# Performance work log

Measured on AMD Instinct MI355X. Metric: run time of the kernel, lower is better.

## Reference

```python
import jax, jax.numpy as jnp
import numpy as np

B, N, F, H, HEADS = 2, 256, 64, 64, 4
C = HEADS * H  # n_coefficients (coefficients_mlp is Identity => must equal n_heads*hidden)
EPS = 1e-5
INF = 1e5


def _lin(key, fan_in, fan_out, bias=True):
    k1, k2 = jax.random.split(key)
    w = jax.random.normal(k1, (fan_in, fan_out), jnp.float32) * (1.0 / np.sqrt(fan_in))
    if bias:
        b = jax.random.normal(k2, (fan_out,), jnp.float32) * 0.01
        return w, b
    return w


def setup_inputs() -> dict:
    key = jax.random.key(0)
    ks = jax.random.split(key, 16)
    inp = dict(
        h=jax.random.normal(ks[0], (B, N, F), jnp.float32),
        x=jax.random.normal(ks[1], (B, N, 3), jnp.float32),
        v=jax.random.normal(ks[2], (B, N, 3), jnp.float32),
    )
    inp['edge_w1'], inp['edge_b1'] = _lin(ks[3], 2 * F + 1, H)
    inp['edge_w2'], inp['edge_b2'] = _lin(ks[4], H, H)
    inp['sem_w'], inp['sem_b'] = _lin(ks[5], H, HEADS)
    inp['post_w1'], inp['post_b1'] = _lin(ks[6], C, H)
    inp['post_w2'], inp['post_b2'] = _lin(ks[7], H, H)
    inp['node_w1'], inp['node_b1'] = _lin(ks[8], C + H + F, H)
    inp['node_w2'], inp['node_b2'] = _lin(ks[9], H, F)
    inp['vel_w1'], inp['vel_b1'] = _lin(ks[10], F, H)
    inp['vel_w2'] = _lin(ks[11], H, 1, bias=False) * 0.001  # xavier gain=0.001 analogue
    inp['vmix_w'] = _lin(ks[12], C, 1, bias=False)[:, 0]
    inp['log_gamma'] = -jnp.log(jnp.linspace(1.0, 5.0, HEADS)).astype(jnp.float32)
    return inp


def reference(h, x, v, edge_w1, edge_b1, edge_w2, edge_b2, sem_w, sem_b,
              post_w1, post_b1, post_w2, post_b2, node_w1, node_b1,
              node_w2, node_b2, vel_w1, vel_b1, vel_w2, vmix_w, log_gamma):
    silu = jax.nn.silu
    n = h.shape[-2]
    eye = jnp.eye(n, dtype=h.dtype)[:, :, None]  # [N,N,1] diagonal mask

    # pairwise geometry: entry [i,j] = x_j - x_i
    x_minus_xt = x[..., None, :, :] - x[..., :, None, :]                # [B,N,N,3]
    x_norm = jnp.sqrt((x_minus_xt ** 2).sum(-1, keepdims=True) + EPS)   # [B,N,N,1]

    # pairwise node-feature concat (h_j, h_i) + distance -> edge MLP
    h_j = jnp.broadcast_to(h[..., None, :, :], (B, n, n, F))
    h_i = jnp.broadcast_to(h[..., :, None, :], (B, n, n, F))
    h_cat = jnp.concatenate([h_j, h_i, x_norm], axis=-1)                # [B,N,N,2F+1]
    h_e_mtx = silu(silu(h_cat @ edge_w1 + edge_b1) @ edge_w2 + edge_b2)  # [B,N,N,H]

    # euclidean attention: softmin over j of gamma*dist, diagonal masked out
    dist = (x_norm + INF * eye) * jnp.exp(log_gamma)                    # [B,N,N,heads]
    euclid_att = jax.nn.softmax(-dist, axis=-2)
    # semantic attention: LeakyReLU(0.2) logits, diagonal masked, softmax over j
    sem = jax.nn.leaky_relu(h_e_mtx @ sem_w + sem_b, 0.2) - INF * eye
    sem_att = jax.nn.softmax(sem, axis=-2)
    comb_att = jax.nn.softmax(euclid_att * sem_att, axis=-2)            # [B,N,N,heads]

    # attention-weighted edge features, flattened over (H, heads)
    h_e_att = (h_e_mtx[..., :, None] * comb_att[..., None, :]).reshape(B, n, n, C)

    # spatial attention (coefficients_mlp is Identity)
    unit = x_minus_xt / (x_norm + EPS)                                  # [B,N,N,3]
    # combinations.mean(dim=-3) without materializing [B,N,N,C,3]
    comb_sum = jnp.einsum('bijc,bijd->bicd', h_e_att, unit) / n         # [B,N,C,3]
    comb_norm = (comb_sum ** 2).sum(-1)                                 # [B,N,C]
    h_comb = silu(silu(comb_norm @ post_w1 + post_b1) @ post_w2 + post_b2)

    # delta_v = mean_j (v_mixing over C of combinations)
    delta_v = jnp.einsum('bijc,c,bijd->bid', h_e_att, vmix_w, unit) / n  # [B,N,3]

    h_agg = h_e_att.sum(axis=-2)                                        # sum over j -> [B,N,C]
    out = jnp.concatenate([h, h_agg, h_comb], axis=-1)
    out = silu(silu(out @ node_w1 + node_b1) @ node_w2 + node_b2)
    h_new = h + out                                                     # residual

    # coordinate / velocity update
    v_scale = silu(h_new @ vel_w1 + vel_b1) @ vel_w2                    # [B,N,1]
    v_new = delta_v + v_scale * v
    x_new = x + v_new
    return h_new, x_new, v_new
```

## Files before the change

### kernel.cpp

```cpp
#include <hip/hip_runtime.h>
#include <hip/hip_bf16.h>
#include <math.h>

#define EPSV 1e-5f
#define INFV 1e5f

typedef short bf16x8 __attribute__((ext_vector_type(8)));
typedef float f32x4 __attribute__((ext_vector_type(4)));

__device__ __forceinline__ float rcp_f(float x) { return __builtin_amdgcn_rcpf(x); }
__device__ __forceinline__ float silu_f(float v) { return v * rcp_f(1.0f + __expf(-v)); }

__device__ __forceinline__ unsigned short f2bf(float f) {
  unsigned int u = __float_as_uint(f);
  u = (u + 0x7fffu + ((u >> 16) & 1u)) >> 16;
  return (unsigned short)u;
}
__device__ __forceinline__ float bf2f(unsigned short h) {
  return __uint_as_float(((unsigned int)h) << 16);
}
__device__ __forceinline__ unsigned int pkbf(float a, float b) {
  float2 f2; f2.x = a; f2.y = b;
  __hip_bfloat162 t = __float22bfloat162_rn(f2);
  unsigned int u;
  __builtin_memcpy(&u, &t, 4);
  return u;
}

__device__ __forceinline__ float4 br4(float4 v, int op, float4* sc) {
  const int tid = threadIdx.x;
#pragma unroll
  for (int off = 32; off >= 1; off >>= 1) {
    float ox = __shfl_xor(v.x, off);
    float oy = __shfl_xor(v.y, off);
    float oz = __shfl_xor(v.z, off);
    float ow = __shfl_xor(v.w, off);
    if (op) { v.x = fmaxf(v.x, ox); v.y = fmaxf(v.y, oy); v.z = fmaxf(v.z, oz); v.w = fmaxf(v.w, ow); }
    else    { v.x += ox; v.y += oy; v.z += oz; v.w += ow; }
  }
  if ((tid & 63) == 0) sc[tid >> 6] = v;
  __syncthreads();
  float4 r0 = sc[0], r1 = sc[1], r2 = sc[2], r3 = sc[3];
  if (op) {
    v.x = fmaxf(fmaxf(r0.x, r1.x), fmaxf(r2.x, r3.x));
    v.y = fmaxf(fmaxf(r0.y, r1.y), fmaxf(r2.y, r3.y));
    v.z = fmaxf(fmaxf(r0.z, r1.z), fmaxf(r2.z, r3.z));
    v.w = fmaxf(fmaxf(r0.w, r1.w), fmaxf(r2.w, r3.w));
  } else {
    v.x = r0.x + r1.x + r2.x + r3.x;
    v.y = r0.y + r1.y + r2.y + r3.y;
    v.z = r0.z + r1.z + r2.z + r3.z;
    v.w = r0.w + r1.w + r2.w + r3.w;
  }
  __syncthreads();
  return v;
}

__device__ __forceinline__ void gemm64(const unsigned short* TH, const unsigned short* E2T,
                                       int w, int l15, int quad, f32x4 acc[4][4]) {
#pragma unroll
  for (int tr = 0; tr < 4; ++tr)
#pragma unroll
    for (int tc = 0; tc < 4; ++tc)
      acc[tr][tc] = (f32x4){0.f, 0.f, 0.f, 0.f};
#pragma unroll
  for (int ms = 0; ms < 64; ms += 32) {
    bf16x8 af[4], bfr[4];
#pragma unroll
    for (int tr = 0; tr < 4; ++tr)
      af[tr] = *reinterpret_cast<const bf16x8*>(&TH[(64 * w + 16 * tr + l15) * 72 + ms + quad * 8]);
#pragma unroll
    for (int tc = 0; tc < 4; ++tc)
      bfr[tc] = *reinterpret_cast<const bf16x8*>(&E2T[(16 * tc + l15) * 72 + ms + quad * 8]);
#pragma unroll
    for (int tr = 0; tr < 4; ++tr)
#pragma unroll
      for (int tc = 0; tc < 4; ++tc)
        acc[tr][tc] = __builtin_amdgcn_mfma_f32_16x16x32_bf16(af[tr], bfr[tc], acc[tr][tc], 0, 0, 0);
  }
}

__global__ __launch_bounds__(256, 3) void k_all(
    const float* __restrict__ h, const float* __restrict__ x, const float* __restrict__ v,
    const float* __restrict__ ew1, const float* __restrict__ eb1,
    const float* __restrict__ ew2, const float* __restrict__ eb2,
    const float* __restrict__ semw, const float* __restrict__ semb,
    const float* __restrict__ pw1, const float* __restrict__ pb1,
    const float* __restrict__ pw2, const float* __restrict__ pb2,
    const float* __restrict__ nw1, const float* __restrict__ nb1,
    const float* __restrict__ nw2, const float* __restrict__ nb2,
    const float* __restrict__ vw1, const float* __restrict__ vb1,
    const float* __restrict__ vw2, const float* __restrict__ vmix,
    const float* __restrict__ lgam, float* __restrict__ out) {

  __shared__ __align__(16) unsigned short TH[256 * 72];
  __shared__ __align__(16) char E2u[9216];
  __shared__ __align__(16) float4 unit_l[256];
  __shared__ float addk[64];
  __shared__ float w1dk[64];
  __shared__ __align__(16) float bms[256];

  unsigned short* E2T = (unsigned short*)E2u;
  float*  sd    = (float*)E2u;
  float4* cat_l = (float4*)E2u;
  float*  cn_l  = (float*)(E2u + 4096);
  float*  hag_l = (float*)(E2u + 5120);
  float4* sc    = (float4*)(E2u + 8192);
  float*  dvs   = (float*)(E2u + 8320);
  float* tmp = (float*)TH;
  float* m1s = (float*)TH + 256;
  float* hnw = (float*)TH + 320;
  float* nin = (float*)TH + 384;

  const int bi  = blockIdx.x;
  const int i   = bi & 255;
  const int b0  = bi & ~255;
  const int tid = threadIdx.x;
  const int j   = tid;
  const int bj  = b0 | j;

  const float xi0 = x[bi * 3 + 0], xi1 = x[bi * 3 + 1], xi2 = x[bi * 3 + 2];
  const float dx = x[bj * 3 + 0] - xi0;
  const float dy = x[bj * 3 + 1] - xi1;
  const float dz = x[bj * 3 + 2] - xi2;
  const float dn = sqrtf(dx * dx + dy * dy + dz * dz + EPSV);
  const float invn = rcp_f(dn + EPSV);
  const float ux = dx * invn, uy = dy * invn, uz = dz * invn;
  unit_l[j] = make_float4(ux, uy, uz, dn);

  {
    const float4* hb4 = reinterpret_cast<const float4*>(h + (size_t)b0 * 64);
#pragma unroll
    for (int q = 0; q < 16; ++q) {
      int idx = q * 256 + tid;
      float4 f4 = hb4[idx];
      int row = idx >> 4, c4 = idx & 15;
      uint2 pk;
      pk.x = pkbf(f4.x, f4.y);
      pk.y = pkbf(f4.z, f4.w);
      *reinterpret_cast<uint2*>(&TH[row * 72 + c4 * 4]) = pk;
    }
  }
#pragma unroll
  for (int q = 0; q < 16; ++q) {
    int idx = q * 256 + tid;
    E2T[(idx & 63) * 72 + (idx >> 6)] = f2bf(ew1[idx]);
  }
  {
    int s = tid >> 6, k = tid & 63;
    const float* hrow = h + (size_t)bi * 64;
    float bp = 0.f;
#pragma unroll
    for (int f2 = 0; f2 < 16; ++f2) {
      int f = s * 16 + f2;
      bp += hrow[f] * ew1[(64 + f) * 64 + k];
    }
    bms[s * 64 + k] = bp;
  }
  __syncthreads();
  if (tid < 64) {
    addk[tid] = eb1[tid] + bms[tid] + bms[64 + tid] + bms[128 + tid] + bms[192 + tid];
    w1dk[tid] = ew1[128 * 64 + tid];
  }

  const int lid  = tid & 63;
  const int w    = tid >> 6;
  const int l15  = lid & 15;
  const int quad = lid >> 4;

  f32x4 acc[4][4];
  gemm64(TH, E2T, w, l15, quad, acc);
  __syncthreads();

#pragma unroll
  for (int tc = 0; tc < 4; ++tc) {
    float ak = addk[16 * tc + l15];
    float wd = w1dk[16 * tc + l15];
#pragma unroll
    for (int tr = 0; tr < 4; ++tr)
#pragma unroll
      for (int r = 0; r < 4; ++r) {
        int row = 64 * w + 16 * tr + quad * 4 + r;
        float val = silu_f(acc[tr][tc][r] + ak + unit_l[row].w * wd);
        TH[row * 72 + 16 * tc + l15] = f2bf(val);
      }
  }
#pragma unroll
  for (int q = 0; q < 16; ++q) {
    int idx = q * 256 + tid;
    E2T[(idx & 63) * 72 + (idx >> 6)] = f2bf(ew2[idx]);
  }
  __syncthreads();

  gemm64(TH, E2T, w, l15, quad, acc);
  __syncthreads();

#pragma unroll
  for (int tc = 0; tc < 4; ++tc) {
    float b2 = eb2[16 * tc + l15];
#pragma unroll
    for (int tr = 0; tr < 4; ++tr)
#pragma unroll
      for (int r = 0; r < 4; ++r) {
        int row = 64 * w + 16 * tr + quad * 4 + r;
        TH[row * 72 + 16 * tc + l15] = f2bf(silu_f(acc[tr][tc][r] + b2));
      }
  }
#pragma unroll
  for (int q = 0; q < 2; ++q) {
    int idx = q * 256 + tid;
    int n = idx >> 6, kk = idx & 63;
    float wv = (n < 4) ? semw[kk * 4 + n] : vmix[kk * 4 + (n - 4)];
    E2T[n * 72 + kk] = f2bf(wv);
  }
  __syncthreads();

  f32x4 acc3[4];
  {
#pragma unroll
    for (int tr = 0; tr < 4; ++tr) acc3[tr] = (f32x4){0.f, 0.f, 0.f, 0.f};
#pragma unroll
    for (int ms = 0; ms < 64; ms += 32) {
      bf16x8 b3 = *reinterpret_cast<const bf16x8*>(&E2T[l15 * 72 + ms + quad * 8]);
#pragma unroll
      for (int tr = 0; tr < 4; ++tr) {
        bf16x8 a3 = *reinterpret_cast<const bf16x8*>(&TH[(64 * w + 16 * tr + l15) * 72 + ms + quad * 8]);
        acc3[tr] = __builtin_amdgcn_mfma_f32_16x16x32_bf16(a3, b3, acc3[tr], 0, 0, 0);
      }
    }
  }
  __syncthreads();
  if (l15 < 8) {
#pragma unroll
    for (int tr = 0; tr < 4; ++tr)
#pragma unroll
      for (int r = 0; r < 4; ++r)
        sd[(64 * w + 16 * tr + quad * 4 + r) * 8 + l15] = acc3[tr][r];
  }
  __syncthreads();

  float4 s01 = *reinterpret_cast<const float4*>(sd + j * 8);
  float4 s23 = *reinterpret_cast<const float4*>(sd + j * 8 + 4);
  float4 sbv = *reinterpret_cast<const float4*>(semb);
  const float diag = (j == i) ? INFV : 0.0f;
  float4 sl;
  sl.x = s01.x + sbv.x; sl.y = s01.y + sbv.y; sl.z = s01.z + sbv.z; sl.w = s01.w + sbv.w;
  sl.x = ((sl.x > 0.f) ? sl.x : 0.2f * sl.x) - diag;
  sl.y = ((sl.y > 0.f) ? sl.y : 0.2f * sl.y) - diag;
  sl.z = ((sl.z > 0.f) ? sl.z : 0.2f * sl.z) - diag;
  sl.w = ((sl.w > 0.f) ? sl.w : 0.2f * sl.w) - diag;

  float4 lg = *reinterpret_cast<const float4*>(lgam);
  const float dni = dn + diag;
  float4 e_eu = make_float4(__expf(-dni * __expf(lg.x)), __expf(-dni * __expf(lg.y)),
                            __expf(-dni * __expf(lg.z)), __expf(-dni * __expf(lg.w)));

  float4 M = br4(sl, 1, sc);
  float4 e_sem = make_float4(__expf(sl.x - M.x), __expf(sl.y - M.y),
                             __expf(sl.z - M.z), __expf(sl.w - M.w));

  float4 a8 = e_eu, b8 = e_sem;
#pragma unroll
  for (int off = 32; off >= 1; off >>= 1) {
    a8.x += __shfl_xor(a8.x, off); a8.y += __shfl_xor(a8.y, off);
    a8.z += __shfl_xor(a8.z, off); a8.w += __shfl_xor(a8.w, off);
    b8.x += __shfl_xor(b8.x, off); b8.y += __shfl_xor(b8.y, off);
    b8.z += __shfl_xor(b8.z, off); b8.w += __shfl_xor(b8.w, off);
  }
  if ((tid & 63) == 0) { sc[tid >> 6] = a8; sc[4 + (tid >> 6)] = b8; }
  __syncthreads();
  float4 Se, Ss;
  {
    float4 r0 = sc[0], r1 = sc[1], r2 = sc[2], r3 = sc[3];
    Se = make_float4(r0.x + r1.x + r2.x + r3.x, r0.y + r1.y + r2.y + r3.y,
                     r0.z + r1.z + r2.z + r3.z, r0.w + r1.w + r2.w + r3.w);
    float4 s0 = sc[4], s1 = sc[5], s2 = sc[6], s3 = sc[7];
    Ss = make_float4(s0.x + s1.x + s2.x + s3.x, s0.y + s1.y + s2.y + s3.y,
                     s0.z + s1.z + s2.z + s3.z, s0.w + s1.w + s2.w + s3.w);
  }
  __syncthreads();

  float4 p = make_float4((e_eu.x * rcp_f(Se.x)) * (e_sem.x * rcp_f(Ss.x)),
                         (e_eu.y * rcp_f(Se.y)) * (e_sem.y * rcp_f(Ss.y)),
                         (e_eu.z * rcp_f(Se.z)) * (e_sem.z * rcp_f(Ss.z)),
                         (e_eu.w * rcp_f(Se.w)) * (e_sem.w * rcp_f(Ss.w)));
  float4 ep = make_float4(__expf(p.x), __expf(p.y), __expf(p.z), __expf(p.w));
  float4 Sp = br4(ep, 0, sc);
  float4 catt = make_float4(ep.x * rcp_f(Sp.x), ep.y * rcp_f(Sp.y),
                            ep.z * rcp_f(Sp.z), ep.w * rcp_f(Sp.w));
  cat_l[j] = catt;

  float s = catt.x * s23.x + catt.y * s23.y + catt.z * s23.z + catt.w * s23.w;
  float4 dv = br4(make_float4(s * ux, s * uy, s * uz, 0.f), 0, sc);
  if (j == 0) {
    const float inv = 1.0f / 256.0f;
    dvs[0] = dv.x * inv; dvs[1] = dv.y * inv; dvs[2] = dv.z * inv;
  }

  {
    const int kk = lid & 15;
    const int jq = lid >> 4;
    const int k  = 16 * w + kk;
    float agg[4] = {0.f, 0.f, 0.f, 0.f};
    float ax[4]  = {0.f, 0.f, 0.f, 0.f};
    float ay[4]  = {0.f, 0.f, 0.f, 0.f};
    float az[4]  = {0.f, 0.f, 0.f, 0.f};
#pragma unroll 4
    for (int jr2 = 0; jr2 < 64; ++jr2) {
      int jj = jq * 64 + ((jr2 + 4 * jq) & 63);
      float hev = bf2f(TH[jj * 72 + k]);
      float4 ca = cat_l[jj];
      float4 u  = unit_l[jj];
      float w0 = hev * ca.x, w1 = hev * ca.y, w2 = hev * ca.z, w3 = hev * ca.w;
      agg[0] += w0; agg[1] += w1; agg[2] += w2; agg[3] += w3;
      ax[0] += w0 * u.x; ay[0] += w0 * u.y; az[0] += w0 * u.z;
      ax[1] += w1 * u.x; ay[1] += w1 * u.y; az[1] += w1 * u.z;
      ax[2] += w2 * u.x; ay[2] += w2 * u.y; az[2] += w2 * u.z;
      ax[3] += w3 * u.x; ay[3] += w3 * u.y; az[3] += w3 * u.z;
    }
#pragma unroll
    for (int off = 16; off <= 32; off <<= 1) {
#pragma unroll
      for (int hd = 0; hd < 4; ++hd) {
        agg[hd] += __shfl_xor(agg[hd], off);
        ax[hd]  += __shfl_xor(ax[hd], off);
        ay[hd]  += __shfl_xor(ay[hd], off);
        az[hd]  += __shfl_xor(az[hd], off);
      }
    }
    if (jq == 0) {
      const float inv = 1.0f / 256.0f;
#pragma unroll
      for (int hd = 0; hd < 4; ++hd) {
        float cx = ax[hd] * inv, cy = ay[hd] * inv, cz = az[hd] * inv;
        cn_l[k * 4 + hd]  = cx * cx + cy * cy + cz * cz;
        hag_l[k * 4 + hd] = agg[hd];
      }
    }
  }
  __syncthreads();

  const int k = tid & 63;
  {
    float a = 0.f;
    for (int m2 = 0; m2 < 64; ++m2) {
      int m = w * 64 + m2;
      a += cn_l[m] * pw1[m * 64 + k];
    }
    tmp[tid] = a;
  }
  __syncthreads();
  if (tid < 64) m1s[tid] = silu_f(pb1[tid] + tmp[tid] + tmp[64 + tid] + tmp[128 + tid] + tmp[192 + tid]);
  __syncthreads();
  {
    float a = 0.f;
#pragma unroll
    for (int m2 = 0; m2 < 16; ++m2) {
      int m = w * 16 + m2;
      a += m1s[m] * pw2[m * 64 + k];
    }
    float hgv = hag_l[tid];
    __syncthreads();
    tmp[tid] = a;
    nin[64 + tid] = hgv;
  }
  __syncthreads();
  if (tid < 64) {
    nin[tid] = h[(size_t)bi * 64 + tid];
    nin[320 + tid] = silu_f(pb2[tid] + tmp[tid] + tmp[64 + tid] + tmp[128 + tid] + tmp[192 + tid]);
  }
  __syncthreads();
  {
    float a = 0.f;
    for (int m2 = 0; m2 < 96; ++m2) {
      int m = w * 96 + m2;
      a += nin[m] * nw1[m * 64 + k];
    }
    __syncthreads();
    tmp[tid] = a;
  }
  __syncthreads();
  if (tid < 64) m1s[tid] = silu_f(nb1[tid] + tmp[tid] + tmp[64 + tid] + tmp[128 + tid] + tmp[192 + tid]);
  __syncthreads();
  {
    float a = 0.f;
#pragma unroll
    for (int m2 = 0; m2 < 16; ++m2) {
      int m = w * 16 + m2;
      a += m1s[m] * nw2[m * 64 + k];
    }
    __syncthreads();
    tmp[tid] = a;
  }
  __syncthreads();
  if (tid < 64) {
    float hn = h[(size_t)bi * 64 + tid] +
               silu_f(nb2[tid] + tmp[tid] + tmp[64 + tid] + tmp[128 + tid] + tmp[192 + tid]);
    out[(size_t)bi * 64 + tid] = hn;
    hnw[tid] = hn;
  }
  __syncthreads();
  {
    float a = 0.f;
#pragma unroll
    for (int m2 = 0; m2 < 16; ++m2) {
      int m = w * 16 + m2;
      a += hnw[m] * vw1[m * 64 + k];
    }
    __syncthreads();
    tmp[tid] = a;
  }
  __syncthreads();
  if (tid < 64) {
    float vh = silu_f(vb1[tid] + tmp[tid] + tmp[64 + tid] + tmp[128 + tid] + tmp[192 + tid]) * vw2[tid];
#pragma unroll
    for (int off = 32; off >= 1; off >>= 1) vh += __shfl_xor(vh, off);
    if (tid == 0) {
#pragma unroll
      for (int d = 0; d < 3; ++d) {
        float vn = dvs[d] + vh * v[bi * 3 + d];
        out[32768 + bi * 3 + d] = x[bi * 3 + d] + vn;
        out[34304 + bi * 3 + d] = vn;
      }
    }
  }
}

extern "C" void kernel_launch(void* const* d_in, const int* in_sizes, int n_in,
                              void* d_out, int out_size, void* d_ws, size_t ws_size,
                              hipStream_t stream) {
  const float* h    = (const float*)d_in[0];
  const float* x    = (const float*)d_in[1];
  const float* v    = (const float*)d_in[2];
  const float* ew1  = (const float*)d_in[3];
  const float* eb1  = (const float*)d_in[4];
  const float* ew2  = (const float*)d_in[5];
  const float* eb2  = (const float*)d_in[6];
  const float* semw = (const float*)d_in[7];
  const float* semb = (const float*)d_in[8];
  const float* pw1  = (const float*)d_in[9];
  const float* pb1  = (const float*)d_in[10];
  const float* pw2  = (const float*)d_in[11];
  const float* pb2  = (const float*)d_in[12];
  const float* nw1  = (const float*)d_in[13];
  const float* nb1  = (const float*)d_in[14];
  const float* nw2  = (const float*)d_in[15];
  const float* nb2  = (const float*)d_in[16];
  const float* vw1  = (const float*)d_in[17];
  const float* vb1  = (const float*)d_in[18];
  const float* vw2  = (const float*)d_in[19];
  const float* vmix = (const float*)d_in[20];
  const float* lgam = (const float*)d_in[21];
  float* out = (float*)d_out;

  k_all<<<512, 256, 0, stream>>>(h, x, v, ew1, eb1, ew2, eb2, semw, semb,
                                 pw1, pb1, pw2, pb2, nw1, nb1, nw2, nb2,
                                 vw1, vb1, vw2, vmix, lgam, out);
}
```

Before: 125.3 us.

## Cut block barriers in softmax reductions and run tail MLPs on one wave

The semantic softmax no longer subtracts a block-wide max, which removes one full block reduction. Each remaining reduction gets its own scratch slot, so several __syncthreads calls can be dropped, including the one between the sem-logit MFMA and the scatter into shared memory. The post, node and velocity MLP tail now runs entirely on wave 0 with no block barriers, instead of being split across four waves with partial-sum merges. The risks are possible exp overflow for large logits, a shared-memory overlap race between the relocated sd buffer and E2T reads, and a longer serial tail on a single wave.

```diff
diff --git a/kernel.cpp b/kernel.cpp
--- a/kernel.cpp
+++ b/kernel.cpp
@@ -25,35 +25,6 @@
   unsigned int u;
   __builtin_memcpy(&u, &t, 4);
   return u;
-}
-
-__device__ __forceinline__ float4 br4(float4 v, int op, float4* sc) {
-  const int tid = threadIdx.x;
-#pragma unroll
-  for (int off = 32; off >= 1; off >>= 1) {
-    float ox = __shfl_xor(v.x, off);
-    float oy = __shfl_xor(v.y, off);
-    float oz = __shfl_xor(v.z, off);
-    float ow = __shfl_xor(v.w, off);
-    if (op) { v.x = fmaxf(v.x, ox); v.y = fmaxf(v.y, oy); v.z = fmaxf(v.z, oz); v.w = fmaxf(v.w, ow); }
-    else    { v.x += ox; v.y += oy; v.z += oz; v.w += ow; }
-  }
-  if ((tid & 63) == 0) sc[tid >> 6] = v;
-  __syncthreads();
-  float4 r0 = sc[0], r1 = sc[1], r2 = sc[2], r3 = sc[3];
-  if (op) {
-    v.x = fmaxf(fmaxf(r0.x, r1.x), fmaxf(r2.x, r3.x));
-    v.y = fmaxf(fmaxf(r0.y, r1.y), fmaxf(r2.y, r3.y));
-    v.z = fmaxf(fmaxf(r0.z, r1.z), fmaxf(r2.z, r3.z));
-    v.w = fmaxf(fmaxf(r0.w, r1.w), fmaxf(r2.w, r3.w));
-  } else {
-    v.x = r0.x + r1.x + r2.x + r3.x;
-    v.y = r0.y + r1.y + r2.y + r3.y;
-    v.z = r0.z + r1.z + r2.z + r3.z;
-    v.w = r0.w + r1.w + r2.w + r3.w;
-  }
-  __syncthreads();
-  return v;
 }
 
 __device__ __forceinline__ void gemm64(const unsigned short* TH, const unsigned short* E2T,
@@ -94,23 +65,21 @@
     const float* __restrict__ lgam, float* __restrict__ out) {
 
   __shared__ __align__(16) unsigned short TH[256 * 72];
-  __shared__ __align__(16) char E2u[9216];
+  __shared__ __align__(16) char E2u[9472];
   __shared__ __align__(16) float4 unit_l[256];
   __shared__ float addk[64];
   __shared__ float w1dk[64];
   __shared__ __align__(16) float bms[256];
 
   unsigned short* E2T = (unsigned short*)E2u;
-  float*  sd    = (float*)E2u;
+  float*  sd    = (float*)(E2u + 1280);
   float4* cat_l = (float4*)E2u;
   float*  cn_l  = (float*)(E2u + 4096);
   float*  hag_l = (float*)(E2u + 5120);
-  float4* sc    = (float4*)(E2u + 8192);
-  float*  dvs   = (float*)(E2u + 8320);
-  float* tmp = (float*)TH;
-  float* m1s = (float*)TH + 256;
-  float* hnw = (float*)TH + 320;
-  float* nin = (float*)TH + 384;
+  float4* scS = (float4*)bms;
+  float4* scP = (float4*)bms + 8;
+  float4* scD = (float4*)bms + 12;
+  float*  dvs = bms + 64;
 
   const int bi  = blockIdx.x;
   const int i   = bi & 255;
@@ -229,7 +198,6 @@
       }
     }
   }
-  __syncthreads();
   if (l15 < 8) {
 #pragma unroll
     for (int tr = 0; tr < 4; ++tr)
@@ -254,10 +222,7 @@
   const float dni = dn + diag;
   float4 e_eu = make_float4(__expf(-dni * __expf(lg.x)), __expf(-dni * __expf(lg.y)),
                             __expf(-dni * __expf(lg.z)), __expf(-dni * __expf(lg.w)));
-
-  float4 M = br4(sl, 1, sc);
-  float4 e_sem = make_float4(__expf(sl.x - M.x), __expf(sl.y - M.y),
-                             __expf(sl.z - M.z), __expf(sl.w - M.w));
+  float4 e_sem = make_float4(__expf(sl.x), __expf(sl.y), __expf(sl.z), __expf(sl.w));
 
   float4 a8 = e_eu, b8 = e_sem;
 #pragma unroll
@@ -267,34 +232,55 @@
     b8.x += __shfl_xor(b8.x, off); b8.y += __shfl_xor(b8.y, off);
     b8.z += __shfl_xor(b8.z, off); b8.w += __shfl_xor(b8.w, off);
   }
-  if ((tid & 63) == 0) { sc[tid >> 6] = a8; sc[4 + (tid >> 6)] = b8; }
+  if (lid == 0) { scS[w] = a8; scS[4 + w] = b8; }
   __syncthreads();
   float4 Se, Ss;
   {
-    float4 r0 = sc[0], r1 = sc[1], r2 = sc[2], r3 = sc[3];
+    float4 r0 = scS[0], r1 = scS[1], r2 = scS[2], r3 = scS[3];
     Se = make_float4(r0.x + r1.x + r2.x + r3.x, r0.y + r1.y + r2.y + r3.y,
                      r0.z + r1.z + r2.z + r3.z, r0.w + r1.w + r2.w + r3.w);
-    float4 s0 = sc[4], s1 = sc[5], s2 = sc[6], s3 = sc[7];
+    float4 s0 = scS[4], s1 = scS[5], s2 = scS[6], s3 = scS[7];
     Ss = make_float4(s0.x + s1.x + s2.x + s3.x, s0.y + s1.y + s2.y + s3.y,
                      s0.z + s1.z + s2.z + s3.z, s0.w + s1.w + s2.w + s3.w);
   }
-  __syncthreads();
 
   float4 p = make_float4((e_eu.x * rcp_f(Se.x)) * (e_sem.x * rcp_f(Ss.x)),
                          (e_eu.y * rcp_f(Se.y)) * (e_sem.y * rcp_f(Ss.y)),
                          (e_eu.z * rcp_f(Se.z)) * (e_sem.z * rcp_f(Ss.z)),
                          (e_eu.w * rcp_f(Se.w)) * (e_sem.w * rcp_f(Ss.w)));
   float4 ep = make_float4(__expf(p.x), __expf(p.y), __expf(p.z), __expf(p.w));
-  float4 Sp = br4(ep, 0, sc);
+  float4 sp8 = ep;
+#pragma unroll
+  for (int off = 32; off >= 1; off >>= 1) {
+    sp8.x += __shfl_xor(sp8.x, off); sp8.y += __shfl_xor(sp8.y, off);
+    sp8.z += __shfl_xor(sp8.z, off); sp8.w += __shfl_xor(sp8.w, off);
+  }
+  if (lid == 0) scP[w] = sp8;
+  __syncthreads();
+  float4 Sp;
+  {
+    float4 r0 = scP[0], r1 = scP[1], r2 = scP[2], r3 = scP[3];
+    Sp = make_float4(r0.x + r1.x + r2.x + r3.x, r0.y + r1.y + r2.y + r3.y,
+                     r0.z + r1.z + r2.z + r3.z, r0.w + r1.w + r2.w + r3.w);
+  }
   float4 catt = make_float4(ep.x * rcp_f(Sp.x), ep.y * rcp_f(Sp.y),
                             ep.z * rcp_f(Sp.z), ep.w * rcp_f(Sp.w));
   cat_l[j] = catt;
 
   float s = catt.x * s23.x + catt.y * s23.y + catt.z * s23.z + catt.w * s23.w;
-  float4 dv = br4(make_float4(s * ux, s * uy, s * uz, 0.f), 0, sc);
+  float dvx = s * ux, dvy = s * uy, dvz = s * uz;
+#pragma unroll
+  for (int off = 32; off >= 1; off >>= 1) {
+    dvx += __shfl_xor(dvx, off); dvy += __shfl_xor(dvy, off); dvz += __shfl_xor(dvz, off);
+  }
+  if (lid == 0) scD[w] = make_float4(dvx, dvy, dvz, 0.f);
+  __syncthreads();
   if (j == 0) {
+    float4 r0 = scD[0], r1 = scD[1], r2 = scD[2], r3 = scD[3];
     const float inv = 1.0f / 256.0f;
-    dvs[0] = dv.x * inv; dvs[1] = dv.y * inv; dvs[2] = dv.z * inv;
+    dvs[0] = (r0.x + r1.x + r2.x + r3.x) * inv;
+    dvs[1] = (r0.y + r1.y + r2.y + r3.y) * inv;
+    dvs[2] = (r0.z + r1.z + r2.z + r3.z) * inv;
   }
 
   {
@@ -340,86 +326,54 @@
   }
   __syncthreads();
 
-  const int k = tid & 63;
-  {
+  if (w == 0) {
+    const int k = tid;
+    float* shr = (float*)TH;
+
     float a = 0.f;
-    for (int m2 = 0; m2 < 64; ++m2) {
-      int m = w * 64 + m2;
-      a += cn_l[m] * pw1[m * 64 + k];
-    }
-    tmp[tid] = a;
-  }
-  __syncthreads();
-  if (tid < 64) m1s[tid] = silu_f(pb1[tid] + tmp[tid] + tmp[64 + tid] + tmp[128 + tid] + tmp[192 + tid]);
-  __syncthreads();
-  {
-    float a = 0.f;
-#pragma unroll
-    for (int m2 = 0; m2 < 16; ++m2) {
-      int m = w * 16 + m2;
-      a += m1s[m] * pw2[m * 64 + k];
-    }
-    float hgv = hag_l[tid];
-    __syncthreads();
-    tmp[tid] = a;
-    nin[64 + tid] = hgv;
-  }
-  __syncthreads();
-  if (tid < 64) {
-    nin[tid] = h[(size_t)bi * 64 + tid];
-    nin[320 + tid] = silu_f(pb2[tid] + tmp[tid] + tmp[64 + tid] + tmp[128 + tid] + tmp[192 + tid]);
-  }
-  __syncthreads();
-  {
-    float a = 0.f;
-    for (int m2 = 0; m2 < 96; ++m2) {
-      int m = w * 96 + m2;
-      a += nin[m] * nw1[m * 64 + k];
-    }
-    __syncthreads();
-    tmp[tid] = a;
-  }
-  __syncthreads();
-  if (tid < 64) m1s[tid] = silu_f(nb1[tid] + tmp[tid] + tmp[64 + tid] + tmp[128 + tid] + tmp[192 + tid]);
-  __syncthreads();
-  {
-    float a = 0.f;
-#pragma unroll
-    for (int m2 = 0; m2 < 16; ++m2) {
-      int m = w * 16 + m2;
-      a += m1s[m] * nw2[m * 64 + k];
-    }
-    __syncthreads();
-    tmp[tid] = a;
-  }
-  __syncthreads();
-  if (tid < 64) {
-    float hn = h[(size_t)bi * 64 + tid] +
-               silu_f(nb2[tid] + tmp[tid] + tmp[64 + tid] + tmp[128 + tid] + tmp[192 + tid]);
-    out[(size_t)bi * 64 + tid] = hn;
-    hnw[tid] = hn;
-  }
-  __syncthreads();
-  {
-    float a = 0.f;
-#pragma unroll
-    for (int m2 = 0; m2 < 16; ++m2) {
-      int m = w * 16 + m2;
-      a += hnw[m] * vw1[m * 64 + k];
-    }
-    __syncthreads();
-    tmp[tid] = a;
-  }
-  __syncthreads();
-  if (tid < 64) {
-    float vh = silu_f(vb1[tid] + tmp[tid] + tmp[64 + tid] + tmp[128 + tid] + tmp[192 + tid]) * vw2[tid];
+#pragma unroll 16
+    for (int m = 0; m < 256; ++m) a += cn_l[m] * pw1[m * 64 + k];
+    float m1 = silu_f(pb1[k] + a);
+    shr[k] = m1;
+
+    a = 0.f;
+#pragma unroll 16
+    for (int m = 0; m < 64; ++m) a += shr[m] * pw2[m * 64 + k];
+    float hcomb = silu_f(pb2[k] + a);
+    float hrow = h[(size_t)bi * 64 + k];
+    shr[64 + k]  = hrow;
+    shr[128 + k] = hcomb;
+
+    a = 0.f;
+#pragma unroll 16
+    for (int m = 0; m < 64; ++m) a += shr[64 + m] * nw1[m * 64 + k];
+#pragma unroll 16
+    for (int m = 0; m < 256; ++m) a += hag_l[m] * nw1[(64 + m) * 64 + k];
+#pragma unroll 16
+    for (int m = 0; m < 64; ++m) a += shr[128 + m] * nw1[(320 + m) * 64 + k];
+    float n1 = silu_f(nb1[k] + a);
+    shr[192 + k] = n1;
+
+    a = 0.f;
+#pragma unroll 16
+    for (int m = 0; m < 64; ++m) a += shr[192 + m] * nw2[m * 64 + k];
+    float hn = hrow + silu_f(nb2[k] + a);
+    out[(size_t)bi * 64 + k] = hn;
+    shr[256 + k] = hn;
+
+    a = 0.f;
+#pragma unroll 16
+    for (int m = 0; m < 64; ++m) a += shr[256 + m] * vw1[m * 64 + k];
+    float vh = silu_f(vb1[k] + a) * vw2[k];
 #pragma unroll
     for (int off = 32; off >= 1; off >>= 1) vh += __shfl_xor(vh, off);
-    if (tid == 0) {
+
+    if (k == 0) {
+      const float xi[3] = {xi0, xi1, xi2};
 #pragma unroll
       for (int d = 0; d < 3; ++d) {
         float vn = dvs[d] + vh * v[bi * 3 + d];
-        out[32768 + bi * 3 + d] = x[bi * 3 + d] + vn;
+        out[32768 + bi * 3 + d] = xi[d] + vn;
         out[34304 + bi * 3 + d] = vn;
       }
     }
```

Measured after the change: 128.4 us. 2.5% more time.
